# Kernel tuning notes

Hardware: AMD Instinct MI355X
Metric: run time of the kernel (lower is better)

Reference implementation:

```python
import jax, jax.numpy as jnp
import numpy as np

K = 20
NEG = 0.2      # leaky relu slope
EPS = 1e-5     # layernorm eps


def knn(x, k=K):
    # x: [B, C, N] -> neighbor indices [B, N, k] by largest negative sq-distance
    xt = jnp.swapaxes(x, 1, 2)                      # [B, N, C]
    inner = -2.0 * jnp.einsum('bnc,bcm->bnm', xt, x)
    xx = jnp.sum(x * x, axis=1)                     # [B, N]
    pd = -xx[:, :, None] - inner - xx[:, None, :]   # [B, N, N]
    _, idx = jax.lax.top_k(pd, k)
    return idx


def graph_feature(x, k=K):
    # x: [B, C, N] -> edge features [B, 2C, N, k] = cat(neighbor - center, center)
    xt = jnp.swapaxes(x, 1, 2)                      # [B, N, C]
    idx = knn(x, k)                                 # [B, N, k]
    nbr = jax.vmap(lambda f, i: f[i])(xt, idx)      # [B, N, k, C]
    ctr = jnp.broadcast_to(xt[:, :, None, :], nbr.shape)
    feat = jnp.concatenate([nbr - ctr, ctr], axis=-1)
    return jnp.transpose(feat, (0, 3, 1, 2))


def lrelu(x):
    return jnp.where(x >= 0, x, NEG * x)


def conv1x1(x, w):
    # x: [B, C, N, k], w: [O, C]  (BatchNorm2d in eval with default stats == identity)
    return jnp.einsum('oc,bcnk->bonk', w, x)


def layernorm(x, g, b):
    m = jnp.mean(x, axis=-1, keepdims=True)
    v = jnp.var(x, axis=-1, keepdims=True)
    return (x - m) * jax.lax.rsqrt(v + EPS) * g + b


def l2n(x):
    return x / jnp.linalg.norm(x, axis=1, keepdims=True)


def fc_layer(x, w, bias, g, beta):
    # l2-normalize -> Linear -> LayerNorm -> LeakyReLU (fc_layer with norm=True, bn=True)
    x = l2n(x)
    x = x @ w.T
    if bias is not None:
        x = x + bias
    return lrelu(layernorm(x, g, beta))


def transform_net(f0, tw1, tw2, tw3, tfc1_w, tfc1_g, tfc1_b, tfc2_w, tfc2_bias, tfc2_g, tfc2_b, tfc3_w, tfc3_b):
    # f0: [B, 6, N, k]
    h = lrelu(conv1x1(f0, tw1))                     # [B, 64, N, k]
    h = lrelu(conv1x1(h, tw2))                      # [B, 128, N, k]
    h = jnp.max(h, axis=-1, keepdims=True)          # [B, 128, N, 1]
    h = lrelu(conv1x1(h, tw3))                      # [B, 1024, N, 1]
    h = jnp.max(h, axis=2)[:, :, 0]                 # [B, 1024]
    h = fc_layer(h, tfc1_w, None, tfc1_g, tfc1_b)   # dgcnn: fc1 bias=False
    h = fc_layer(h, tfc2_w, tfc2_bias, tfc2_g, tfc2_b)
    h = h @ tfc3_w.T + tfc3_b                       # [B, 9]
    h = h + jnp.eye(3, dtype=h.dtype).reshape(9)
    return h.reshape(-1, 3, 3)


def setup_inputs() -> dict:
    key = jax.random.key(0)
    ks = jax.random.split(key, 16)

    def w(k, o, i):
        return jax.random.normal(k, (o, i), dtype=jnp.float32) / np.sqrt(i)

    inp = {
        'x': jax.random.normal(ks[0], (16, 3, 1024), dtype=jnp.float32),
        # transform_net params
        'tw1': w(ks[1], 64, 6),
        'tw2': w(ks[2], 128, 64),
        'tw3': w(ks[3], 1024, 128),
        'tfc1_w': w(ks[4], 512, 1024),
        'tfc1_g': jnp.ones((512,), jnp.float32),
        'tfc1_b': jnp.zeros((512,), jnp.float32),
        'tfc2_w': w(ks[5], 256, 512),
        'tfc2_bias': jnp.zeros((256,), jnp.float32),
        'tfc2_g': jnp.ones((256,), jnp.float32),
        'tfc2_b': jnp.zeros((256,), jnp.float32),
        'tfc3_w': w(ks[6], 9, 256) * 0.01,
        'tfc3_b': jnp.zeros((9,), jnp.float32),
        # EdgeConv params (1x1 convs, bias=False for dgcnn)
        'w1': w(ks[7], 64, 6),
        'w2': w(ks[8], 64, 128),
        'w3': w(ks[9], 128, 128),
        'w4': w(ks[10], 256, 256),
        'w5': w(ks[11], 1024, 512),
    }
    return inp


def reference(x, tw1, tw2, tw3, tfc1_w, tfc1_g, tfc1_b, tfc2_w, tfc2_bias, tfc2_g, tfc2_b,
              tfc3_w, tfc3_b, w1, w2, w3, w4, w5):
    # spatial transform from first graph feature
    f0 = graph_feature(x)                           # [B, 6, N, k]
    t = transform_net(f0, tw1, tw2, tw3, tfc1_w, tfc1_g, tfc1_b,
                      tfc2_w, tfc2_bias, tfc2_g, tfc2_b, tfc3_w, tfc3_b)
    x = jnp.einsum('bij,bjn->bin', t, x)            # [B, 3, N]

    # 4 EdgeConv blocks: graph_feature -> 1x1 conv (+BN identity) -> lrelu -> max over k
    x1 = jnp.max(lrelu(conv1x1(graph_feature(x), w1)), axis=-1)    # [B, 64, N]
    x2 = jnp.max(lrelu(conv1x1(graph_feature(x1), w2)), axis=-1)   # [B, 64, N]
    x3 = jnp.max(lrelu(conv1x1(graph_feature(x2), w3)), axis=-1)   # [B, 128, N]
    x4 = jnp.max(lrelu(conv1x1(graph_feature(x3), w4)), axis=-1)   # [B, 256, N]

    xc = jnp.concatenate([x1, x2, x3, x4], axis=1)  # [B, 512, N]
    x5 = lrelu(jnp.einsum('oc,bcn->bon', w5, xc))   # [B, 1024, N]
    return jnp.max(x5, axis=-1)                     # [B, 1024] global feature
```

## Files before the change

### kernel.cpp

```cpp
#include <hip/hip_runtime.h>
#include <math.h>

#define BATCH 16
#define NPTS 1024
#define KNN 20

__device__ __forceinline__ float lrelu(float v) { return v >= 0.f ? v : 0.2f * v; }

typedef __attribute__((ext_vector_type(8))) short bf16x8;
typedef __attribute__((ext_vector_type(4))) float f32x4;
typedef unsigned long long ull;

__device__ __forceinline__ ushort f2bf(float f) {
  union { float f; unsigned u; } v; v.f = f;
  unsigned r = (v.u + 0x7FFFu + ((v.u >> 16) & 1u)) >> 16;
  return (ushort)r;
}

__device__ __forceinline__ unsigned wave_min_u32(unsigned v) {
  unsigned t;
  t = (unsigned)__builtin_amdgcn_update_dpp((int)v, (int)v, 0x111, 0xf, 0xf, false);
  v = t < v ? t : v;
  t = (unsigned)__builtin_amdgcn_update_dpp((int)v, (int)v, 0x112, 0xf, 0xf, false);
  v = t < v ? t : v;
  t = (unsigned)__builtin_amdgcn_update_dpp((int)v, (int)v, 0x114, 0xf, 0xf, false);
  v = t < v ? t : v;
  t = (unsigned)__builtin_amdgcn_update_dpp((int)v, (int)v, 0x118, 0xf, 0xf, false);
  v = t < v ? t : v;
  t = (unsigned)__builtin_amdgcn_update_dpp((int)v, (int)v, 0x142, 0xf, 0xf, false);
  v = t < v ? t : v;
  t = (unsigned)__builtin_amdgcn_update_dpp((int)v, (int)v, 0x143, 0xf, 0xf, false);
  v = t < v ? t : v;
  return (unsigned)__builtin_amdgcn_readlane((int)v, 63);
}

__global__ __launch_bounds__(256)
void wsplit_t_kernel(const float* __restrict__ W, float* __restrict__ waT,
                     float* __restrict__ wdT, int O, int Cc) {
  int e = blockIdx.x * 256 + threadIdx.x;
  if (e < O * Cc) {
    int c = e / O, o = e - c * O;
    float a = W[o * 2 * Cc + c], bb = W[o * 2 * Cc + Cc + c];
    waT[e] = a; wdT[e] = bb - a;
  }
}

__global__ __launch_bounds__(256)
void wsplit_bf_kernel(const float* __restrict__ W, ushort* __restrict__ wa_bf,
                      ushort* __restrict__ wd_bf, int O, int Cc) {
  int e = blockIdx.x * 256 + threadIdx.x;
  if (e < O * Cc) {
    int o = e / Cc, c = e - o * Cc;
    float a = W[o * 2 * Cc + c], bb = W[o * 2 * Cc + Cc + c];
    wa_bf[e] = f2bf(a); wd_bf[e] = f2bf(bb - a);
  }
}

__global__ __launch_bounds__(256)
void cvt_bf16_kernel(const float* __restrict__ in, ushort* __restrict__ outp, int n) {
  int e = blockIdx.x * 256 + threadIdx.x;
  if (e < n) outp[e] = f2bf(in[e]);
}

__global__ __launch_bounds__(256)
void wtrans_kernel(const float* __restrict__ W, float* __restrict__ wT, int O, int Cc) {
  int e = blockIdx.x * 256 + threadIdx.x;
  if (e < O * Cc) {
    int c = e / O, o = e - c * O;
    wT[e] = W[(size_t)o * Cc + c];
  }
}

__global__ __launch_bounds__(256)
void xx3_kernel(const float* __restrict__ x, float* __restrict__ xx) {
  const int b = blockIdx.y;
  const int n = blockIdx.x * 256 + threadIdx.x;
  const float* xb = x + (size_t)b * 3 * NPTS;
  float a = xb[n], bb = xb[NPTS + n], c = xb[2 * NPTS + n];
  xx[b * NPTS + n] = a * a + bb * bb + c * c;
}

template<int C>
__global__ __launch_bounds__(256)
void knn_cn_kernel(const float* __restrict__ Xt, long sb,
                   const float* __restrict__ xx, int* __restrict__ idxout) {
  __shared__ float sc4[4][NPTS];
  const int b = blockIdx.y, i0 = blockIdx.x * 16;
  const int tid = threadIdx.x;
  const float* Xb = Xt + (size_t)b * sb;
  const int j0 = tid * 4;
  float acc[16][4];
  #pragma unroll
  for (int q = 0; q < 16; ++q)
    #pragma unroll
    for (int u = 0; u < 4; ++u) acc[q][u] = 0.f;
  for (int c = 0; c < C; ++c) {
    const float4 xv = *reinterpret_cast<const float4*>(Xb + (size_t)c * NPTS + j0);
    const float* xr = Xb + (size_t)c * NPTS + i0;
    #pragma unroll
    for (int q = 0; q < 16; ++q) {
      const float xiq = xr[q];
      acc[q][0] = fmaf(xiq, xv.x, acc[q][0]);
      acc[q][1] = fmaf(xiq, xv.y, acc[q][1]);
      acc[q][2] = fmaf(xiq, xv.z, acc[q][2]);
      acc[q][3] = fmaf(xiq, xv.w, acc[q][3]);
    }
  }
  const float4 xxj = *reinterpret_cast<const float4*>(xx + b * NPTS + j0);
  const int wv = tid >> 6, lane = tid & 63;
  unsigned ku[4][16];

  #pragma unroll
  for (int r = 0; r < 4; ++r) {
    if (r > 0) __syncthreads();
    #pragma unroll
    for (int q = 0; q < 4; ++q) {
      const int qq = r * 4 + q;
      float4 st;
      st.x = fmaf(-2.f, acc[qq][0], xxj.x);
      st.y = fmaf(-2.f, acc[qq][1], xxj.y);
      st.z = fmaf(-2.f, acc[qq][2], xxj.z);
      st.w = fmaf(-2.f, acc[qq][3], xxj.w);
      *reinterpret_cast<float4*>(&sc4[q][j0]) = st;
    }
    __syncthreads();
    #pragma unroll
    for (int s = 0; s < 16; ++s) {
      const unsigned u = __float_as_uint(sc4[wv][lane + 64 * s]);
      ku[r][s] = u ^ ((unsigned)((int)u >> 31) | 0x80000000u);
    }
  }

  unsigned c1s[4], c2s[4]; int c1j[4], c2j[4];
  #pragma unroll
  for (int r = 0; r < 4; ++r) {
    unsigned b1 = 0xFFFFFFFFu, b2 = 0xFFFFFFFFu; int s1 = 0, s2 = 0;
    #pragma unroll
    for (int s = 0; s < 16; ++s) {
      const unsigned k = ku[r][s];
      const bool a1 = k < b1, a2 = k < b2;
      const unsigned n1 = a1 ? k : b1;  const int ns1 = a1 ? s : s1;
      const unsigned n2 = a1 ? b1 : (a2 ? k : b2);
      const int ns2 = a1 ? s1 : (a2 ? s : s2);
      b1 = n1; s1 = ns1; b2 = n2; s2 = ns2;
    }
    c1s[r] = b1; c1j[r] = lane + (s1 << 6);
    c2s[r] = b2; c2j[r] = lane + (s2 << 6);
  }
  const unsigned INVS = 0xFFFFFFFFu;
  int my[4] = {0, 0, 0, 0};
  for (int t = 0; t < KNN; ++t) {
    unsigned ws[4]; int wl[4], jw[4];
    #pragma unroll
    for (int r = 0; r < 4; ++r) ws[r] = wave_min_u32(c1s[r]);
    #pragma unroll
    for (int r = 0; r < 4; ++r) wl[r] = __ffsll((long long)__ballot(c1s[r] == ws[r])) - 1;
    #pragma unroll
    for (int r = 0; r < 4; ++r) jw[r] = __builtin_amdgcn_readlane(c1j[r], wl[r]);
    if (lane == t) {
      #pragma unroll
      for (int r = 0; r < 4; ++r) my[r] = jw[r];
    }
    bool cons = false;
    #pragma unroll
    for (int r = 0; r < 4; ++r) {
      const bool win = (lane == wl[r]);
      c1s[r] = win ? c2s[r] : c1s[r];
      c1j[r] = win ? c2j[r] : c1j[r];
      c2s[r] = win ? INVS : c2s[r];
      cons = cons || (c1s[r] == INVS);
    }
    if (__any(cons)) {
      #pragma unroll
      for (int r = 0; r < 4; ++r) {
        if (c1s[r] == INVS) {
          unsigned m1 = INVS, m2 = INVS; int r1 = 0, r2 = 0;
          #pragma unroll
          for (int s = 0; s < 16; ++s) {
            const unsigned k = ku[r][s];
            const bool ok = k > ws[r];
            const bool a1 = ok && (k < m1), a2 = ok && (k < m2);
            const unsigned nm1 = a1 ? k : m1;  const int nr1 = a1 ? s : r1;
            const unsigned nm2 = a1 ? m1 : (a2 ? k : m2);
            const int nr2 = a1 ? r1 : (a2 ? s : r2);
            m1 = nm1; r1 = nr1; m2 = nm2; r2 = nr2;
          }
          c1s[r] = (m1 == INVS) ? 0xFFFFFFFEu : m1;  c1j[r] = lane + (r1 << 6);
          c2s[r] = (m2 == INVS) ? 0xFFFFFFFEu : m2;  c2j[r] = lane + (r2 << 6);
        }
      }
    }
  }
  if (lane < KNN) {
    #pragma unroll
    for (int r = 0; r < 4; ++r)
      idxout[(size_t)(b * NPTS + i0 + r * 4 + wv) * KNN + lane] = my[r];
  }
}

__global__ __launch_bounds__(256)
void gemm_dual_kernel(const float* __restrict__ X, long sxb, int sxn, int sxc,
                      const float* __restrict__ WaT, const float* __restrict__ WdT,
                      int ldW, int C,
                      float* __restrict__ outY, float* __restrict__ outZ,
                      int sob, int son) {
  __shared__ __align__(16) float Xs[16][64];
  __shared__ __align__(16) float Was[16][64];
  __shared__ __align__(16) float Wds[16][64];
  const int b = blockIdx.z;
  const int n0 = blockIdx.x * 64, o0 = blockIdx.y * 64;
  const int tid = threadIdx.x;
  const int lr = tid & 63;
  const int c4 = (tid >> 6) * 4;
  const int tn = tid & 15, to = tid >> 4;
  float accY[4][4], accZ[4][4];
  #pragma unroll
  for (int i = 0; i < 4; ++i)
    #pragma unroll
    for (int j = 0; j < 4; ++j) { accY[i][j] = 0.f; accZ[i][j] = 0.f; }

  const size_t xbase = (size_t)b * sxb;
  for (int k0 = 0; k0 < C; k0 += 16) {
    #pragma unroll
    for (int u = 0; u < 4; ++u) {
      int c = k0 + c4 + u;
      float xv = 0.f, wa = 0.f, wd = 0.f;
      if (c < C) {
        xv = X[xbase + (size_t)(n0 + lr) * sxn + (size_t)c * sxc];
        wa = WaT[(size_t)c * ldW + o0 + lr];
        wd = WdT[(size_t)c * ldW + o0 + lr];
      }
      Xs[c4 + u][lr] = xv;
      Was[c4 + u][lr] = wa;
      Wds[c4 + u][lr] = wd;
    }
    __syncthreads();
    #pragma unroll
    for (int kk = 0; kk < 16; ++kk) {
      const float4 xa = *reinterpret_cast<const float4*>(&Xs[kk][tn * 4]);
      const float4 wav = *reinterpret_cast<const float4*>(&Was[kk][to * 4]);
      const float4 wdv = *reinterpret_cast<const float4*>(&Wds[kk][to * 4]);
      const float xr[4] = {xa.x, xa.y, xa.z, xa.w};
      const float war[4] = {wav.x, wav.y, wav.z, wav.w};
      const float wdr[4] = {wdv.x, wdv.y, wdv.z, wdv.w};
      #pragma unroll
      for (int i = 0; i < 4; ++i)
        #pragma unroll
        for (int j = 0; j < 4; ++j) {
          accY[i][j] = fmaf(xr[i], war[j], accY[i][j]);
          accZ[i][j] = fmaf(xr[i], wdr[j], accZ[i][j]);
        }
    }
    __syncthreads();
  }
  #pragma unroll
  for (int i = 0; i < 4; ++i) {
    const size_t base = (size_t)b * sob + (size_t)(n0 + tn * 4 + i) * son + o0 + to * 4;
    *reinterpret_cast<float4*>(&outY[base]) =
      make_float4(accY[i][0], accY[i][1], accY[i][2], accY[i][3]);
    *reinterpret_cast<float4*>(&outZ[base]) =
      make_float4(accZ[i][0], accZ[i][1], accZ[i][2], accZ[i][3]);
  }
}

template<int EPI>
__global__ __launch_bounds__(256)
void gemm128_kernel(const float* __restrict__ X, long sxb, int scN,
                    const float* __restrict__ WT, int ldW, int C,
                    float* __restrict__ out, int sob, int son, int snb) {
  __shared__ __align__(16) float Xs[16][128];
  __shared__ __align__(16) float Ws[16][128];
  __shared__ __align__(16) float red[16][132];
  const int b = blockIdx.z;
  const int n0 = blockIdx.x * 128, o0 = blockIdx.y * 128;
  const int tid = threadIdx.x;
  const int tn = tid & 15, to = tid >> 4;
  float acc[8][8];
  #pragma unroll
  for (int i = 0; i < 8; ++i)
    #pragma unroll
    for (int j = 0; j < 8; ++j) acc[i][j] = 0.f;

  const size_t xbase = (size_t)b * sxb;
  for (int c0 = 0; c0 < C; c0 += 16) {
    #pragma unroll
    for (int it = 0; it < 2; ++it) {
      const int task = tid + it * 256;
      const int kk = task >> 5, n4 = (task & 31) * 4;
      *reinterpret_cast<float4*>(&Xs[kk][n4]) =
        *reinterpret_cast<const float4*>(&X[xbase + (size_t)(c0 + kk) * scN + n0 + n4]);
      *reinterpret_cast<float4*>(&Ws[kk][n4]) =
        *reinterpret_cast<const float4*>(&WT[(size_t)(c0 + kk) * ldW + o0 + n4]);
    }
    __syncthreads();
    #pragma unroll
    for (int kk = 0; kk < 16; ++kk) {
      const float4 xa0 = *reinterpret_cast<const float4*>(&Xs[kk][tn * 4]);
      const float4 xa1 = *reinterpret_cast<const float4*>(&Xs[kk][64 + tn * 4]);
      const float4 wb0 = *reinterpret_cast<const float4*>(&Ws[kk][to * 4]);
      const float4 wb1 = *reinterpret_cast<const float4*>(&Ws[kk][64 + to * 4]);
      const float xr[8] = {xa0.x, xa0.y, xa0.z, xa0.w, xa1.x, xa1.y, xa1.z, xa1.w};
      const float wr[8] = {wb0.x, wb0.y, wb0.z, wb0.w, wb1.x, wb1.y, wb1.z, wb1.w};
      #pragma unroll
      for (int i = 0; i < 8; ++i)
        #pragma unroll
        for (int j = 0; j < 8; ++j) acc[i][j] = fmaf(xr[i], wr[j], acc[i][j]);
    }
    __syncthreads();
  }

  if (EPI == 0) {
    #pragma unroll
    for (int i = 0; i < 8; ++i) {
      const int n = n0 + (i >> 2) * 64 + tn * 4 + (i & 3);
      float4 s0 = make_float4(acc[i][0], acc[i][1], acc[i][2], acc[i][3]);
      float4 s1 = make_float4(acc[i][4], acc[i][5], acc[i][6], acc[i][7]);
      *reinterpret_cast<float4*>(&out[(size_t)b * sob + (size_t)n * son + o0 + to * 4]) = s0;
      *reinterpret_cast<float4*>(&out[(size_t)b * sob + (size_t)n * son + o0 + 64 + to * 4]) = s1;
    }
  } else {
    #pragma unroll
    for (int j = 0; j < 8; ++j) {
      float m = lrelu(acc[0][j]);
      #pragma unroll
      for (int i = 1; i < 8; ++i) m = fmaxf(m, lrelu(acc[i][j]));
      red[tn][(j >> 2) * 64 + to * 4 + (j & 3)] = m;
    }
    __syncthreads();
    if (tid < 128) {
      float m = red[0][tid];
      #pragma unroll
      for (int t = 1; t < 16; ++t) m = fmaxf(m, red[t][tid]);
      out[(size_t)b * sob + (size_t)blockIdx.x * snb + o0 + tid] = m;
    }
  }
}

template<int EPI>
__global__ __launch_bounds__(256)
void gemm_mfma_kernel(const ushort* __restrict__ Xg, long sxb, int ldX,
                      const ushort* __restrict__ Wg, int ldW, int K,
                      float* __restrict__ out, long sob, int son, int snb) {
  __shared__ __align__(16) ushort As[128 * 64];
  __shared__ __align__(16) ushort Bs[128 * 64];
// ... 295 lines not shown
  }
  a2 = a2 * rinv2 + bias2[tid];
  float mean2 = block_reduce_sum(a2, rbuf) * (1.f / 256.f);
  float dd = a2 - mean2;
  float var2 = block_reduce_sum(dd * dd, rbuf) * (1.f / 256.f);
  float rs2 = 1.0f / sqrtf(var2 + 1e-5f);
  f2s[tid] = lrelu((a2 - mean2) * rs2 * g2[tid] + bb2[tid]);
  __syncthreads();
  if (tid < 9) {
    const float* wrow3 = Wt3 + tid * 256;
    float a3 = 0.f;
    for (int c = 0; c < 256; ++c) a3 = fmaf(wrow3[c], f2s[c], a3);
    a3 += bb3[tid];
    if (tid == 0 || tid == 4 || tid == 8) a3 += 1.f;
    tm[tid] = a3;
  }
  __syncthreads();
  const float* xb = x + (size_t)b * 3 * NPTS;
  float* ob = xt + (size_t)b * 3 * NPTS;
  #pragma unroll
  for (int nt = 0; nt < 4; ++nt) {
    const int n = nt * 256 + tid;
    const float x0 = xb[n], x1 = xb[NPTS + n], x2 = xb[2 * NPTS + n];
    #pragma unroll
    for (int i = 0; i < 3; ++i)
      ob[i * NPTS + n] = fmaf(tm[3 * i], x0, fmaf(tm[3 * i + 1], x1, tm[3 * i + 2] * x2));
  }
}

extern "C" void kernel_launch(void* const* d_in, const int* in_sizes, int n_in,
                              void* d_out, int out_size, void* d_ws, size_t ws_size,
                              hipStream_t stream) {
  (void)in_sizes; (void)n_in; (void)out_size; (void)ws_size;
  const float* x       = (const float*)d_in[0];
  const float* tw1     = (const float*)d_in[1];
  const float* tw2     = (const float*)d_in[2];
  const float* tw3     = (const float*)d_in[3];
  const float* tfc1_w  = (const float*)d_in[4];
  const float* tfc1_g  = (const float*)d_in[5];
  const float* tfc1_b  = (const float*)d_in[6];
  const float* tfc2_w  = (const float*)d_in[7];
  const float* tfc2_bias = (const float*)d_in[8];
  const float* tfc2_g  = (const float*)d_in[9];
  const float* tfc2_b  = (const float*)d_in[10];
  const float* tfc3_w  = (const float*)d_in[11];
  const float* tfc3_b  = (const float*)d_in[12];
  const float* w1      = (const float*)d_in[13];
  const float* w2      = (const float*)d_in[14];
  const float* w3      = (const float*)d_in[15];
  const float* w4      = (const float*)d_in[16];
  const float* w5      = (const float*)d_in[17];
  float* out = (float*)d_out;

  char* wsb = (char*)d_ws;
  size_t off = 0;
  auto alloc = [&](size_t bytes) -> void* {
    void* p = wsb + off;
    off += (bytes + 255) & ~(size_t)255;
    return p;
  };
  float* ybuf = (float*)alloc((size_t)BATCH * NPTS * 256 * 4);
  float* zbuf = (float*)alloc((size_t)BATCH * NPTS * 256 * 4);
  float* xcT  = (float*)alloc((size_t)BATCH * 512 * NPTS * 4);
  ushort* xc_bf = (ushort*)alloc((size_t)BATCH * NPTS * 512 * 2);
  float* h2m  = (float*)alloc((size_t)BATCH * 128 * NPTS * 4);
  float* part = (float*)alloc((size_t)BATCH * 16 * 1024 * 4);
  int*   idxb = (int*)alloc((size_t)BATCH * NPTS * KNN * 4);
  float* xxb  = (float*)alloc((size_t)BATCH * NPTS * 4);
  float* xt   = (float*)alloc((size_t)BATCH * 3 * NPTS * 4);
  float* tw1aT = (float*)alloc(3 * 64 * 4);
  float* tw1dT = (float*)alloc(3 * 64 * 4);
  float* w1aT  = (float*)alloc(3 * 64 * 4);
  float* w1dT  = (float*)alloc(3 * 64 * 4);
  float* w2aT  = (float*)alloc(64 * 64 * 4);
  float* w2dT  = (float*)alloc(64 * 64 * 4);
  float* w3aT  = (float*)alloc(64 * 128 * 4);
  float* w3dT  = (float*)alloc(64 * 128 * 4);
  ushort* w4a_bf = (ushort*)alloc(256 * 128 * 2);
  ushort* w4d_bf = (ushort*)alloc(256 * 128 * 2);
  ushort* w5_bf  = (ushort*)alloc(1024 * 512 * 2);
  float* tw2T  = (float*)alloc(64 * 128 * 4);
  float* tw3T  = (float*)alloc(128 * 1024 * 4);

  wsplit_t_kernel<<<1, 256, 0, stream>>>(tw1, tw1aT, tw1dT, 64, 3);
  wsplit_t_kernel<<<1, 256, 0, stream>>>(w1, w1aT, w1dT, 64, 3);
  wsplit_t_kernel<<<16, 256, 0, stream>>>(w2, w2aT, w2dT, 64, 64);
  wsplit_t_kernel<<<32, 256, 0, stream>>>(w3, w3aT, w3dT, 128, 64);
  wsplit_bf_kernel<<<128, 256, 0, stream>>>(w4, w4a_bf, w4d_bf, 256, 128);
  cvt_bf16_kernel<<<2048, 256, 0, stream>>>(w5, w5_bf, 1024 * 512);
  wtrans_kernel<<<32, 256, 0, stream>>>(tw2, tw2T, 128, 64);
  wtrans_kernel<<<512, 256, 0, stream>>>(tw3, tw3T, 1024, 128);

  xx3_kernel<<<dim3(4, 16), 256, 0, stream>>>(x, xxb);
  knn_cn_kernel<3><<<dim3(64, 16), 256, 0, stream>>>(x, 3 * NPTS, xxb, idxb);
  gemm_dual_kernel<<<dim3(16, 1, 16), 256, 0, stream>>>(x, 3 * NPTS, 1, NPTS, tw1aT, tw1dT,
                                                        64, 3, ybuf, zbuf, NPTS * 64, 64);
  h12_gemm_kernel<<<dim3(256, 16), 256, 0, stream>>>(ybuf, zbuf, idxb, tw2T, h2m);
  gemm128_kernel<1><<<dim3(8, 8, 16), 256, 0, stream>>>(h2m, 128 * NPTS, NPTS, tw3T, 1024, 128,
                                                        part, 8 * 1024, 0, 1024);
  fcall_kernel<<<16, 256, 0, stream>>>(part, tfc1_w, tfc1_g, tfc1_b,
                                       tfc2_w, tfc2_bias, tfc2_g, tfc2_b,
                                       tfc3_w, tfc3_b, x, xt);

  xx3_kernel<<<dim3(4, 16), 256, 0, stream>>>(xt, xxb);
  knn_cn_kernel<3><<<dim3(64, 16), 256, 0, stream>>>(xt, 3 * NPTS, xxb, idxb);
  gemm_dual_kernel<<<dim3(16, 1, 16), 256, 0, stream>>>(xt, 3 * NPTS, 1, NPTS, w1aT, w1dT,
                                                        64, 3, ybuf, zbuf, NPTS * 64, 64);
  edge_max_cn_kernel<64, 64><<<dim3(16, 16), 256, 0, stream>>>(ybuf, zbuf, idxb, xcT, xxb,
                                                               xc_bf, 0);

  knn_cn_kernel<64><<<dim3(64, 16), 256, 0, stream>>>(xcT, 512 * NPTS, xxb, idxb);
  gemm_dual_kernel<<<dim3(16, 1, 16), 256, 0, stream>>>(xcT, 512 * NPTS, 1, NPTS, w2aT, w2dT,
                                                        64, 64, ybuf, zbuf, NPTS * 64, 64);
  edge_max_cn_kernel<64, 64><<<dim3(16, 16), 256, 0, stream>>>(ybuf, zbuf, idxb,
                                                               xcT + 64 * NPTS, xxb, xc_bf, 64);

  knn_cn_kernel<64><<<dim3(64, 16), 256, 0, stream>>>(xcT + 64 * NPTS, 512 * NPTS, xxb, idxb);
  gemm_dual_kernel<<<dim3(16, 2, 16), 256, 0, stream>>>(xcT + 64 * NPTS, 512 * NPTS, 1, NPTS,
                                                        w3aT, w3dT, 128, 64,
                                                        ybuf, zbuf, NPTS * 128, 128);
  edge_max_cn_kernel<128, 64><<<dim3(16, 16), 256, 0, stream>>>(ybuf, zbuf, idxb,
                                                                xcT + 128 * NPTS, xxb, xc_bf, 128);

  knn_cn_kernel<128><<<dim3(64, 16), 256, 0, stream>>>(xcT + 128 * NPTS, 512 * NPTS, xxb, idxb);
  gemm_mfma_kernel<0><<<dim3(8, 2, 16), 256, 0, stream>>>(xc_bf + 128, (long)NPTS * 512, 512,
                                                          w4a_bf, 128, 128,
                                                          ybuf, (long)NPTS * 256, 256, 0);
  gemm_mfma_kernel<0><<<dim3(8, 2, 16), 256, 0, stream>>>(xc_bf + 128, (long)NPTS * 512, 512,
                                                          w4d_bf, 128, 128,
                                                          zbuf, (long)NPTS * 256, 256, 0);
  edge_max_cn_kernel<256, 32><<<dim3(32, 16), 256, 0, stream>>>(ybuf, zbuf, idxb,
                                                                xcT + 256 * NPTS, nullptr,
                                                                xc_bf, 256);

  gemm_mfma_kernel<1><<<dim3(8, 8, 16), 256, 0, stream>>>(xc_bf, (long)NPTS * 512, 512,
                                                          w5_bf, 512, 512,
                                                          part, 8 * 1024, 0, 1024);
  reduce_max_kernel<<<dim3(4, 16), 256, 0, stream>>>(part, out, 8);
}
```

Before: 734.9 us.

## Merge kNN and edge GEMM into single launches and fuse weight prep

Eight weight-preparation kernels become one prep_all_kernel. Each kNN launch and its independent dual-weight GEMM now share one launch, with block-index ranges deciding which work a block does, so the two run concurrently and launch count drops. For C=3 the squared norms are computed inside the kNN pass, which removes the xx3 kernels. This aims to cut launch overhead and fill the GPU better with the small GEMM grids, at the cost of heterogeneous blocks sharing one register and LDS allocation sized for the larger path.

Measured after the change: 690.1 us, median of 2. -6.1%, faster.

```diff
diff --git a/kernel.cpp b/kernel.cpp
--- a/kernel.cpp
+++ b/kernel.cpp
@@ -9,7 +9,6 @@
 
 typedef __attribute__((ext_vector_type(8))) short bf16x8;
 typedef __attribute__((ext_vector_type(4))) float f32x4;
-typedef unsigned long long ull;
 
 __device__ __forceinline__ ushort f2bf(float f) {
   union { float f; unsigned u; } v; v.f = f;
@@ -35,231 +34,437 @@
 }
 
 __global__ __launch_bounds__(256)
-void wsplit_t_kernel(const float* __restrict__ W, float* __restrict__ waT,
-                     float* __restrict__ wdT, int O, int Cc) {
-  int e = blockIdx.x * 256 + threadIdx.x;
-  if (e < O * Cc) {
-    int c = e / O, o = e - c * O;
-    float a = W[o * 2 * Cc + c], bb = W[o * 2 * Cc + Cc + c];
-    waT[e] = a; wdT[e] = bb - a;
-  }
-}
-
+void prep_all_kernel(const float* __restrict__ tw1, const float* __restrict__ w1,
+                     const float* __restrict__ w2, const float* __restrict__ w3,
+                     const float* __restrict__ w4, const float* __restrict__ w5,
+                     const float* __restrict__ tw2, const float* __restrict__ tw3,
+                     float* __restrict__ tw1aT, float* __restrict__ tw1dT,
+                     float* __restrict__ w1aT, float* __restrict__ w1dT,
+                     float* __restrict__ w2aT, float* __restrict__ w2dT,
+                     float* __restrict__ w3aT, float* __restrict__ w3dT,
+                     ushort* __restrict__ w4a_bf, ushort* __restrict__ w4d_bf,
+                     ushort* __restrict__ w5_bf,
+                     float* __restrict__ tw2T, float* __restrict__ tw3T) {
+  int g = blockIdx.x * 256 + threadIdx.x;
+  if (g < 524288) { w5_bf[g] = f2bf(w5[g]); return; }
+  g -= 524288;
+  if (g < 131072) { int c = g >> 10, o = g & 1023; tw3T[g] = tw3[o * 128 + c]; return; }
+  g -= 131072;
+  if (g < 32768) {
+    int o = g >> 7, c = g & 127;
+    float a = w4[o * 256 + c], bb = w4[o * 256 + 128 + c];
+    w4a_bf[g] = f2bf(a); w4d_bf[g] = f2bf(bb - a);
+    return;
+  }
+  g -= 32768;
+  if (g < 8192) {
+    int c = g >> 7, o = g & 127;
+    float a = w3[o * 128 + c], bb = w3[o * 128 + 64 + c];
+    w3aT[g] = a; w3dT[g] = bb - a;
+    return;
+  }
+  g -= 8192;
+  if (g < 8192) { int c = g >> 7, o = g & 127; tw2T[g] = tw2[o * 64 + c]; return; }
+  g -= 8192;
+  if (g < 4096) {
+    int c = g >> 6, o = g & 63;
+    float a = w2[o * 128 + c], bb = w2[o * 128 + 64 + c];
+    w2aT[g] = a; w2dT[g] = bb - a;
+    return;
+  }
+  g -= 4096;
+  if (g < 192) {
+    int c = g >> 6, o = g & 63;
+    float a = tw1[o * 6 + c], bb = tw1[o * 6 + 3 + c];
+    tw1aT[g] = a; tw1dT[g] = bb - a;
+    return;
+  }
+  g -= 192;
+  if (g < 192) {
+    int c = g >> 6, o = g & 63;
+    float a = w1[o * 6 + c], bb = w1[o * 6 + 3 + c];
+    w1aT[g] = a; w1dT[g] = bb - a;
+  }
+}
+
+template<int C, int NO>
 __global__ __launch_bounds__(256)
-void wsplit_bf_kernel(const float* __restrict__ W, ushort* __restrict__ wa_bf,
-                      ushort* __restrict__ wd_bf, int O, int Cc) {
-  int e = blockIdx.x * 256 + threadIdx.x;
-  if (e < O * Cc) {
-    int o = e / Cc, c = e - o * Cc;
-    float a = W[o * 2 * Cc + c], bb = W[o * 2 * Cc + Cc + c];
-    wa_bf[e] = f2bf(a); wd_bf[e] = f2bf(bb - a);
+void knn_dual_kernel(const float* __restrict__ X, long sxb,
+                     const float* __restrict__ xx, int* __restrict__ idxout,
+                     const float* __restrict__ WaT, const float* __restrict__ WdT,
+                     int ldW, float* __restrict__ outY, float* __restrict__ outZ,
+                     long sob, int son) {
+  __shared__ __align__(16) char smem[16384];
+  const int gid = blockIdx.x;
+  const int tid = threadIdx.x;
+
+  if (gid < 1024) {
+    float (*sc4)[NPTS] = reinterpret_cast<float (*)[NPTS]>(smem);
+    const int b = gid >> 6, i0 = (gid & 63) * 16;
+    const float* Xb = X + (size_t)b * sxb;
+    const int j0 = tid * 4;
+    float acc[16][4];
+    #pragma unroll
+    for (int q = 0; q < 16; ++q)
+      #pragma unroll
+      for (int u = 0; u < 4; ++u) acc[q][u] = 0.f;
+    float4 xxjv = make_float4(0.f, 0.f, 0.f, 0.f);
+    for (int c = 0; c < C; ++c) {
+      const float4 xv = *reinterpret_cast<const float4*>(Xb + (size_t)c * NPTS + j0);
+      if (C == 3) {
+        xxjv.x = fmaf(xv.x, xv.x, xxjv.x);
+        xxjv.y = fmaf(xv.y, xv.y, xxjv.y);
+        xxjv.z = fmaf(xv.z, xv.z, xxjv.z);
+        xxjv.w = fmaf(xv.w, xv.w, xxjv.w);
+      }
+      const float* xr = Xb + (size_t)c * NPTS + i0;
+      #pragma unroll
+      for (int q = 0; q < 16; ++q) {
+        const float xiq = xr[q];
+        acc[q][0] = fmaf(xiq, xv.x, acc[q][0]);
+        acc[q][1] = fmaf(xiq, xv.y, acc[q][1]);
+        acc[q][2] = fmaf(xiq, xv.z, acc[q][2]);
+        acc[q][3] = fmaf(xiq, xv.w, acc[q][3]);
+      }
+    }
+    float4 xxj;
+    if (C == 3) xxj = xxjv;
+    else xxj = *reinterpret_cast<const float4*>(xx + b * NPTS + j0);
+    const int wv = tid >> 6, lane = tid & 63;
+    unsigned ku[4][16];
+
+    #pragma unroll
+    for (int r = 0; r < 4; ++r) {
+      if (r > 0) __syncthreads();
+      #pragma unroll
+      for (int q = 0; q < 4; ++q) {
+        const int qq = r * 4 + q;
+        float4 st;
+        st.x = fmaf(-2.f, acc[qq][0], xxj.x);
+        st.y = fmaf(-2.f, acc[qq][1], xxj.y);
+        st.z = fmaf(-2.f, acc[qq][2], xxj.z);
+        st.w = fmaf(-2.f, acc[qq][3], xxj.w);
+        *reinterpret_cast<float4*>(&sc4[q][j0]) = st;
+      }
+      __syncthreads();
+      #pragma unroll
+      for (int s = 0; s < 16; ++s) {
+        const unsigned u = __float_as_uint(sc4[wv][lane + 64 * s]);
+        ku[r][s] = u ^ ((unsigned)((int)u >> 31) | 0x80000000u);
+      }
+    }
+
+    unsigned c1s[4], c2s[4]; int c1j[4], c2j[4];
+    #pragma unroll
+    for (int r = 0; r < 4; ++r) {
+      unsigned b1 = 0xFFFFFFFFu, b2 = 0xFFFFFFFFu; int s1 = 0, s2 = 0;
+      #pragma unroll
+      for (int s = 0; s < 16; ++s) {
+        const unsigned k = ku[r][s];
+        const bool a1 = k < b1, a2 = k < b2;
+        const unsigned n1 = a1 ? k : b1;  const int ns1 = a1 ? s : s1;
+        const unsigned n2 = a1 ? b1 : (a2 ? k : b2);
+        const int ns2 = a1 ? s1 : (a2 ? s : s2);
+        b1 = n1; s1 = ns1; b2 = n2; s2 = ns2;
+      }
+      c1s[r] = b1; c1j[r] = lane + (s1 << 6);
+      c2s[r] = b2; c2j[r] = lane + (s2 << 6);
+    }
+    const unsigned INVS = 0xFFFFFFFFu;
+    int my[4] = {0, 0, 0, 0};
+    for (int t = 0; t < KNN; ++t) {
+      unsigned ws[4]; int wl[4], jw[4];
+      #pragma unroll
+      for (int r = 0; r < 4; ++r) ws[r] = wave_min_u32(c1s[r]);
+      #pragma unroll
+      for (int r = 0; r < 4; ++r) wl[r] = __ffsll((long long)__ballot(c1s[r] == ws[r])) - 1;
+      #pragma unroll
+      for (int r = 0; r < 4; ++r) jw[r] = __builtin_amdgcn_readlane(c1j[r], wl[r]);
+      if (lane == t) {
+        #pragma unroll
+        for (int r = 0; r < 4; ++r) my[r] = jw[r];
+      }
+      bool cons = false;
+      #pragma unroll
+      for (int r = 0; r < 4; ++r) {
+        const bool win = (lane == wl[r]);
+        c1s[r] = win ? c2s[r] : c1s[r];
+        c1j[r] = win ? c2j[r] : c1j[r];
+        c2s[r] = win ? INVS : c2s[r];
+        cons = cons || (c1s[r] == INVS);
+      }
+      if (__any(cons)) {
+        #pragma unroll
+        for (int r = 0; r < 4; ++r) {
+          if (c1s[r] == INVS) {
+            unsigned m1 = INVS, m2 = INVS; int r1 = 0, r2 = 0;
+            #pragma unroll
+            for (int s = 0; s < 16; ++s) {
+              const unsigned k = ku[r][s];
+              const bool ok = k > ws[r];
+              const bool a1 = ok && (k < m1), a2 = ok && (k < m2);
+              const unsigned nm1 = a1 ? k : m1;  const int nr1 = a1 ? s : r1;
+              const unsigned nm2 = a1 ? m1 : (a2 ? k : m2);
+              const int nr2 = a1 ? r1 : (a2 ? s : r2);
+              m1 = nm1; r1 = nr1; m2 = nm2; r2 = nr2;
+            }
+            c1s[r] = (m1 == INVS) ? 0xFFFFFFFEu : m1;  c1j[r] = lane + (r1 << 6);
+            c2s[r] = (m2 == INVS) ? 0xFFFFFFFEu : m2;  c2j[r] = lane + (r2 << 6);
+          }
+        }
+      }
+    }
+    if (lane < KNN) {
+      #pragma unroll
+      for (int r = 0; r < 4; ++r)
+        idxout[(size_t)(b * NPTS + i0 + r * 4 + wv) * KNN + lane] = my[r];
+    }
+  } else {
+    float (*Xs)[64]  = reinterpret_cast<float (*)[64]>(smem);
+    float (*Was)[64] = reinterpret_cast<float (*)[64]>(smem + 4096);
+    float (*Wds)[64] = reinterpret_cast<float (*)[64]>(smem + 8192);
+    const int g2 = gid - 1024;
+    const int bx = g2 & 15;
+    const int rest = g2 >> 4;
+    const int oy = rest % NO;
+    const int b = rest / NO;
+    const int n0 = bx * 64, o0 = oy * 64;
+    const int lr = tid & 63;
+    const int c4 = (tid >> 6) * 4;
+    const int tn = tid & 15, to = tid >> 4;
+    float accY[4][4], accZ[4][4];
+    #pragma unroll
+    for (int i = 0; i < 4; ++i)
+      #pragma unroll
+      for (int j = 0; j < 4; ++j) { accY[i][j] = 0.f; accZ[i][j] = 0.f; }
+
+    const size_t xbase = (size_t)b * sxb;
+    for (int k0 = 0; k0 < C; k0 += 16) {
+      #pragma unroll
+      for (int u = 0; u < 4; ++u) {
+        int c = k0 + c4 + u;
+        float xv = 0.f, wa = 0.f, wd = 0.f;
+        if (c < C) {
+          xv = X[xbase + (size_t)(n0 + lr) + (size_t)c * NPTS];
+          wa = WaT[(size_t)c * ldW + o0 + lr];
+          wd = WdT[(size_t)c * ldW + o0 + lr];
+        }
+        Xs[c4 + u][lr] = xv;
+        Was[c4 + u][lr] = wa;
+        Wds[c4 + u][lr] = wd;
+      }
+      __syncthreads();
+      #pragma unroll
+      for (int kk = 0; kk < 16; ++kk) {
+        const float4 xa = *reinterpret_cast<const float4*>(&Xs[kk][tn * 4]);
+        const float4 wav = *reinterpret_cast<const float4*>(&Was[kk][to * 4]);
+        const float4 wdv = *reinterpret_cast<const float4*>(&Wds[kk][to * 4]);
+        const float xr[4] = {xa.x, xa.y, xa.z, xa.w};
+        const float war[4] = {wav.x, wav.y, wav.z, wav.w};
+        const float wdr[4] = {wdv.x, wdv.y, wdv.z, wdv.w};
+        #pragma unroll
+        for (int i = 0; i < 4; ++i)
+          #pragma unroll
+          for (int j = 0; j < 4; ++j) {
+            accY[i][j] = fmaf(xr[i], war[j], accY[i][j]);
+            accZ[i][j] = fmaf(xr[i], wdr[j], accZ[i][j]);
+          }
+      }
+      __syncthreads();
+    }
+    #pragma unroll
+    for (int i = 0; i < 4; ++i) {
+      const size_t base = (size_t)b * sob + (size_t)(n0 + tn * 4 + i) * son + o0 + to * 4;
+      *reinterpret_cast<float4*>(&outY[base]) =
+        make_float4(accY[i][0], accY[i][1], accY[i][2], accY[i][3]);
+      *reinterpret_cast<float4*>(&outZ[base]) =
+        make_float4(accZ[i][0], accZ[i][1], accZ[i][2], accZ[i][3]);
+    }
   }
 }
 
 __global__ __launch_bounds__(256)
-void cvt_bf16_kernel(const float* __restrict__ in, ushort* __restrict__ outp, int n) {
-  int e = blockIdx.x * 256 + threadIdx.x;
-  if (e < n) outp[e] = f2bf(in[e]);
-}
-
-__global__ __launch_bounds__(256)
-void wtrans_kernel(const float* __restrict__ W, float* __restrict__ wT, int O, int Cc) {
-  int e = blockIdx.x * 256 + threadIdx.x;
-  if (e < O * Cc) {
-    int c = e / O, o = e - c * O;
-    wT[e] = W[(size_t)o * Cc + c];
-  }
-}
-
-__global__ __launch_bounds__(256)
-void xx3_kernel(const float* __restrict__ x, float* __restrict__ xx) {
-  const int b = blockIdx.y;
-  const int n = blockIdx.x * 256 + threadIdx.x;
-  const float* xb = x + (size_t)b * 3 * NPTS;
-  float a = xb[n], bb = xb[NPTS + n], c = xb[2 * NPTS + n];
-  xx[b * NPTS + n] = a * a + bb * bb + c * c;
-}
-
-template<int C>
-__global__ __launch_bounds__(256)
-void knn_cn_kernel(const float* __restrict__ Xt, long sb,
-                   const float* __restrict__ xx, int* __restrict__ idxout) {
-  __shared__ float sc4[4][NPTS];
-  const int b = blockIdx.y, i0 = blockIdx.x * 16;
+void knn_mfma_kernel(const float* __restrict__ Xt, long sxb,
+                     const float* __restrict__ xx, int* __restrict__ idxout,
+                     const ushort* __restrict__ Xg,
+                     const ushort* __restrict__ w4a, const ushort* __restrict__ w4d,
+                     float* __restrict__ ybuf, float* __restrict__ zbuf) {
+  __shared__ __align__(16) char smem[32768];
+  const int gid = blockIdx.x;
   const int tid = threadIdx.x;
-  const float* Xb = Xt + (size_t)b * sb;
-  const int j0 = tid * 4;
-  float acc[16][4];
-  #pragma unroll
-  for (int q = 0; q < 16; ++q)
-    #pragma unroll
-    for (int u = 0; u < 4; ++u) acc[q][u] = 0.f;
-  for (int c = 0; c < C; ++c) {
-    const float4 xv = *reinterpret_cast<const float4*>(Xb + (size_t)c * NPTS + j0);
-    const float* xr = Xb + (size_t)c * NPTS + i0;
-    #pragma unroll
-    for (int q = 0; q < 16; ++q) {
-      const float xiq = xr[q];
-      acc[q][0] = fmaf(xiq, xv.x, acc[q][0]);
-      acc[q][1] = fmaf(xiq, xv.y, acc[q][1]);
-      acc[q][2] = fmaf(xiq, xv.z, acc[q][2]);
-      acc[q][3] = fmaf(xiq, xv.w, acc[q][3]);
-    }
-  }
-  const float4 xxj = *reinterpret_cast<const float4*>(xx + b * NPTS + j0);
-  const int wv = tid >> 6, lane = tid & 63;
-  unsigned ku[4][16];
-
-  #pragma unroll
-  for (int r = 0; r < 4; ++r) {
-    if (r > 0) __syncthreads();
-    #pragma unroll
-    for (int q = 0; q < 4; ++q) {
-      const int qq = r * 4 + q;
-      float4 st;
-      st.x = fmaf(-2.f, acc[qq][0], xxj.x);
-      st.y = fmaf(-2.f, acc[qq][1], xxj.y);
-      st.z = fmaf(-2.f, acc[qq][2], xxj.z);
-      st.w = fmaf(-2.f, acc[qq][3], xxj.w);
-      *reinterpret_cast<float4*>(&sc4[q][j0]) = st;
-    }
-    __syncthreads();
-    #pragma unroll
-    for (int s = 0; s < 16; ++s) {
-      const unsigned u = __float_as_uint(sc4[wv][lane + 64 * s]);
-      ku[r][s] = u ^ ((unsigned)((int)u >> 31) | 0x80000000u);
-    }
-  }
-
-  unsigned c1s[4], c2s[4]; int c1j[4], c2j[4];
-  #pragma unroll
-  for (int r = 0; r < 4; ++r) {
-    unsigned b1 = 0xFFFFFFFFu, b2 = 0xFFFFFFFFu; int s1 = 0, s2 = 0;
-    #pragma unroll
-    for (int s = 0; s < 16; ++s) {
-      const unsigned k = ku[r][s];
-      const bool a1 = k < b1, a2 = k < b2;
-      const unsigned n1 = a1 ? k : b1;  const int ns1 = a1 ? s : s1;
-      const unsigned n2 = a1 ? b1 : (a2 ? k : b2);
-      const int ns2 = a1 ? s1 : (a2 ? s : s2);
-      b1 = n1; s1 = ns1; b2 = n2; s2 = ns2;
-    }
-    c1s[r] = b1; c1j[r] = lane + (s1 << 6);
-    c2s[r] = b2; c2j[r] = lane + (s2 << 6);
-  }
-  const unsigned INVS = 0xFFFFFFFFu;
-  int my[4] = {0, 0, 0, 0};
-  for (int t = 0; t < KNN; ++t) {
-    unsigned ws[4]; int wl[4], jw[4];
-    #pragma unroll
-    for (int r = 0; r < 4; ++r) ws[r] = wave_min_u32(c1s[r]);
-    #pragma unroll
-    for (int r = 0; r < 4; ++r) wl[r] = __ffsll((long long)__ballot(c1s[r] == ws[r])) - 1;
-    #pragma unroll
-    for (int r = 0; r < 4; ++r) jw[r] = __builtin_amdgcn_readlane(c1j[r], wl[r]);
-    if (lane == t) {
-      #pragma unroll
-      for (int r = 0; r < 4; ++r) my[r] = jw[r];
-    }
-    bool cons = false;
+
+  if (gid < 1024) {
+    float (*sc4)[NPTS] = reinterpret_cast<float (*)[NPTS]>(smem);
+    const int b = gid >> 6, i0 = (gid & 63) * 16;
+    const float* Xb = Xt + (size_t)b * sxb;
+    const int j0 = tid * 4;
+    float acc[16][4];
+    #pragma unroll
+    for (int q = 0; q < 16; ++q)
+      #pragma unroll
+      for (int u = 0; u < 4; ++u) acc[q][u] = 0.f;
+    for (int c = 0; c < 128; ++c) {
+      const float4 xv = *reinterpret_cast<const float4*>(Xb + (size_t)c * NPTS + j0);
+      const float* xr = Xb + (size_t)c * NPTS + i0;
+      #pragma unroll
+      for (int q = 0; q < 16; ++q) {
+        const float xiq = xr[q];
+        acc[q][0] = fmaf(xiq, xv.x, acc[q][0]);
+        acc[q][1] = fmaf(xiq, xv.y, acc[q][1]);
+        acc[q][2] = fmaf(xiq, xv.z, acc[q][2]);
+        acc[q][3] = fmaf(xiq, xv.w, acc[q][3]);
+      }
+    }
+    const float4 xxj = *reinterpret_cast<const float4*>(xx + b * NPTS + j0);
+    const int wv = tid >> 6, lane = tid & 63;
+    unsigned ku[4][16];
     #pragma unroll
     for (int r = 0; r < 4; ++r) {
-      const bool win = (lane == wl[r]);
-      c1s[r] = win ? c2s[r] : c1s[r];
-      c1j[r] = win ? c2j[r] : c1j[r];
-      c2s[r] = win ? INVS : c2s[r];
-      cons = cons || (c1s[r] == INVS);
-    }
-    if (__any(cons)) {
+      if (r > 0) __syncthreads();
+      #pragma unroll
+      for (int q = 0; q < 4; ++q) {
+        const int qq = r * 4 + q;
+        float4 st;
+        st.x = fmaf(-2.f, acc[qq][0], xxj.x);
+        st.y = fmaf(-2.f, acc[qq][1], xxj.y);
+        st.z = fmaf(-2.f, acc[qq][2], xxj.z);
+        st.w = fmaf(-2.f, acc[qq][3], xxj.w);
+        *reinterpret_cast<float4*>(&sc4[q][j0]) = st;
+      }
+      __syncthreads();
+      #pragma unroll
+      for (int s = 0; s < 16; ++s) {
+        const unsigned u = __float_as_uint(sc4[wv][lane + 64 * s]);
+        ku[r][s] = u ^ ((unsigned)((int)u >> 31) | 0x80000000u);
+      }
+    }
+    unsigned c1s[4], c2s[4]; int c1j[4], c2j[4];
+    #pragma unroll
+    for (int r = 0; r < 4; ++r) {
+      unsigned b1 = 0xFFFFFFFFu, b2 = 0xFFFFFFFFu; int s1 = 0, s2 = 0;
+      #pragma unroll
+      for (int s = 0; s < 16; ++s) {
+        const unsigned k = ku[r][s];
+        const bool a1 = k < b1, a2 = k < b2;
+        const unsigned n1 = a1 ? k : b1;  const int ns1 = a1 ? s : s1;
+        const unsigned n2 = a1 ? b1 : (a2 ? k : b2);
+        const int ns2 = a1 ? s1 : (a2 ? s : s2);
+        b1 = n1; s1 = ns1; b2 = n2; s2 = ns2;
+      }
+      c1s[r] = b1; c1j[r] = lane + (s1 << 6);
+      c2s[r] = b2; c2j[r] = lane + (s2 << 6);
+    }
+    const unsigned INVS = 0xFFFFFFFFu;
+    int my[4] = {0, 0, 0, 0};
+    for (int t = 0; t < KNN; ++t) {
+      unsigned ws[4]; int wl[4], jw[4];
+      #pragma unroll
+      for (int r = 0; r < 4; ++r) ws[r] = wave_min_u32(c1s[r]);
+      #pragma unroll
+      for (int r = 0; r < 4; ++r) wl[r] = __ffsll((long long)__ballot(c1s[r] == ws[r])) - 1;
+      #pragma unroll
+      for (int r = 0; r < 4; ++r) jw[r] = __builtin_amdgcn_readlane(c1j[r], wl[r]);
+      if (lane == t) {
+        #pragma unroll
+        for (int r = 0; r < 4; ++r) my[r] = jw[r];
+      }
+      bool cons = false;
       #pragma unroll
       for (int r = 0; r < 4; ++r) {
-        if (c1s[r] == INVS) {
-          unsigned m1 = INVS, m2 = INVS; int r1 = 0, r2 = 0;
+        const bool win = (lane == wl[r]);
+        c1s[r] = win ? c2s[r] : c1s[r];
+        c1j[r] = win ? c2j[r] : c1j[r];
+        c2s[r] = win ? INVS : c2s[r];
+        cons = cons || (c1s[r] == INVS);
+      }
+      if (__any(cons)) {
+        #pragma unroll
+        for (int r = 0; r < 4; ++r) {
+          if (c1s[r] == INVS) {
+            unsigned m1 = INVS, m2 = INVS; int r1 = 0, r2 = 0;
+            #pragma unroll
+            for (int s = 0; s < 16; ++s) {
+              const unsigned k = ku[r][s];
+              const bool ok = k > ws[r];
+              const bool a1 = ok && (k < m1), a2 = ok && (k < m2);
+              const unsigned nm1 = a1 ? k : m1;  const int nr1 = a1 ? s : r1;
+              const unsigned nm2 = a1 ? m1 : (a2 ? k : m2);
+              const int nr2 = a1 ? r1 : (a2 ? s : r2);
+              m1 = nm1; r1 = nr1; m2 = nm2; r2 = nr2;
+            }
+            c1s[r] = (m1 == INVS) ? 0xFFFFFFFEu : m1;  c1j[r] = lane + (r1 << 6);
+            c2s[r] = (m2 == INVS) ? 0xFFFFFFFEu : m2;  c2j[r] = lane + (r2 << 6);
+          }
+        }
+      }
+    }
+    if (lane < KNN) {
+      #pragma unroll
+      for (int r = 0; r < 4; ++r)
+        idxout[(size_t)(b * NPTS + i0 + r * 4 + wv) * KNN + lane] = my[r];
+    }
+  } else {
+    char* As = smem;
+    char* Bs = smem + 16384;
+    int g2 = gid - 1024;
+    const ushort* Wg = (g2 < 256) ? w4a : w4d;
+    float* outp = (g2 < 256) ? ybuf : zbuf;
+    g2 &= 255;
+    const int bx = g2 & 7, oy = (g2 >> 3) & 1, b = g2 >> 4;
+    const int n0 = bx * 128, o0 = oy * 128;
+    const int lane = tid & 63;
+    const int wrow = (tid >> 6) >> 1, wcol = (tid >> 6) & 1;
+    f32x4 acc[4][4];
+    #pragma unroll
+    for (int i = 0; i < 4; ++i)
+      #pragma unroll
+      for (int j = 0; j < 4; ++j)
+        #pragma unroll
+        for (int r = 0; r < 4; ++r) acc[i][j][r] = 0.f;
+
+    const ushort* Xb = Xg + (size_t)b * NPTS * 512;
+    for (int kb = 0; kb < 128; kb += 64) {
+      #pragma unroll
+      for (int i = 0; i < 4; ++i) {
+        const int idx = i * 256 + tid;
+        const int n = idx >> 3, kc = idx & 7;
+        const bf16x8 xv = *reinterpret_cast<const bf16x8*>(&Xb[(size_t)(n0 + n) * 512 + kb + kc * 8]);
+        const bf16x8 wvv = *reinterpret_cast<const bf16x8*>(&Wg[(size_t)(o0 + n) * 128 + kb + kc * 8]);
+        const int ad = n * 128 + ((kc * 16) ^ ((n & 7) << 4));
+        *reinterpret_cast<bf16x8*>(As + ad) = xv;
+        *reinterpret_cast<bf16x8*>(Bs + ad) = wvv;
+      }
+      __syncthreads();
+      #pragma unroll
+      for (int s = 0; s < 2; ++s) {
+        bf16x8 af[4], bfr[4];
+        const int klane = (s * 64 + ((lane >> 4) << 4));
+        #pragma unroll
+        for (int f = 0; f < 4; ++f) {
+          const int nl = wrow * 64 + f * 16 + (lane & 15);
+          af[f] = *reinterpret_cast<const bf16x8*>(As + nl * 128 + (klane ^ ((nl & 7) << 4)));
+          const int ol = wcol * 64 + f * 16 + (lane & 15);
+          bfr[f] = *reinterpret_cast<const bf16x8*>(Bs + ol * 128 + (klane ^ ((ol & 7) << 4)));
+        }
+        #pragma unroll
+        for (int i = 0; i < 4; ++i)
           #pragma unroll
-          for (int s = 0; s < 16; ++s) {
-            const unsigned k = ku[r][s];
-            const bool ok = k > ws[r];
-            const bool a1 = ok && (k < m1), a2 = ok && (k < m2);
-            const unsigned nm1 = a1 ? k : m1;  const int nr1 = a1 ? s : r1;
-            const unsigned nm2 = a1 ? m1 : (a2 ? k : m2);
-            const int nr2 = a1 ? r1 : (a2 ? s : r2);
-            m1 = nm1; r1 = nr1; m2 = nm2; r2 = nr2;
-          }
-          c1s[r] = (m1 == INVS) ? 0xFFFFFFFEu : m1;  c1j[r] = lane + (r1 << 6);
-          c2s[r] = (m2 == INVS) ? 0xFFFFFFFEu : m2;  c2j[r] = lane + (r2 << 6);
+          for (int j = 0; j < 4; ++j)
+            acc[i][j] = __builtin_amdgcn_mfma_f32_16x16x32_bf16(af[i], bfr[j], acc[i][j], 0, 0, 0);
+      }
+      __syncthreads();
+    }
+    #pragma unroll
+    for (int i = 0; i < 4; ++i)
+      #pragma unroll
+      for (int r = 0; r < 4; ++r) {
+        const int n = n0 + wrow * 64 + i * 16 + ((lane >> 4) << 2) + r;
+        #pragma unroll
+        for (int j = 0; j < 4; ++j) {
+          const int o = o0 + wcol * 64 + j * 16 + (lane & 15);
+          outp[(size_t)b * NPTS * 256 + (size_t)n * 256 + o] = acc[i][j][r];
         }
       }
-    }
-  }
-  if (lane < KNN) {
-    #pragma unroll
-    for (int r = 0; r < 4; ++r)
-      idxout[(size_t)(b * NPTS + i0 + r * 4 + wv) * KNN + lane] = my[r];
-  }
-}
-
-__global__ __launch_bounds__(256)
-void gemm_dual_kernel(const float* __restrict__ X, long sxb, int sxn, int sxc,
-                      const float* __restrict__ WaT, const float* __restrict__ WdT,
-                      int ldW, int C,
-                      float* __restrict__ outY, float* __restrict__ outZ,
-                      int sob, int son) {
-  __shared__ __align__(16) float Xs[16][64];
-  __shared__ __align__(16) float Was[16][64];
-  __shared__ __align__(16) float Wds[16][64];
-  const int b = blockIdx.z;
-  const int n0 = blockIdx.x * 64, o0 = blockIdx.y * 64;
-  const int tid = threadIdx.x;
-  const int lr = tid & 63;
-  const int c4 = (tid >> 6) * 4;
-  const int tn = tid & 15, to = tid >> 4;
-  float accY[4][4], accZ[4][4];
-  #pragma unroll
-  for (int i = 0; i < 4; ++i)
-    #pragma unroll
-    for (int j = 0; j < 4; ++j) { accY[i][j] = 0.f; accZ[i][j] = 0.f; }
-
-  const size_t xbase = (size_t)b * sxb;
-  for (int k0 = 0; k0 < C; k0 += 16) {
-    #pragma unroll
-    for (int u = 0; u < 4; ++u) {
-      int c = k0 + c4 + u;
-      float xv = 0.f, wa = 0.f, wd = 0.f;
-      if (c < C) {
-        xv = X[xbase + (size_t)(n0 + lr) * sxn + (size_t)c * sxc];
-        wa = WaT[(size_t)c * ldW + o0 + lr];
-        wd = WdT[(size_t)c * ldW + o0 + lr];
-      }
-      Xs[c4 + u][lr] = xv;
-      Was[c4 + u][lr] = wa;
-      Wds[c4 + u][lr] = wd;
-    }
-    __syncthreads();
-    #pragma unroll
-    for (int kk = 0; kk < 16; ++kk) {
-      const float4 xa = *reinterpret_cast<const float4*>(&Xs[kk][tn * 4]);
-      const float4 wav = *reinterpret_cast<const float4*>(&Was[kk][to * 4]);
-      const float4 wdv = *reinterpret_cast<const float4*>(&Wds[kk][to * 4]);
-      const float xr[4] = {xa.x, xa.y, xa.z, xa.w};
-      const float war[4] = {wav.x, wav.y, wav.z, wav.w};
-      const float wdr[4] = {wdv.x, wdv.y, wdv.z, wdv.w};
-      #pragma unroll
-      for (int i = 0; i < 4; ++i)
-        #pragma unroll
-        for (int j = 0; j < 4; ++j) {
-          accY[i][j] = fmaf(xr[i], war[j], accY[i][j]);
-          accZ[i][j] = fmaf(xr[i], wdr[j], accZ[i][j]);
-        }
-    }
-    __syncthreads();
-  }
-  #pragma unroll
-  for (int i = 0; i < 4; ++i) {
-    const size_t base = (size_t)b * sob + (size_t)(n0 + tn * 4 + i) * son + o0 + to * 4;
-    *reinterpret_cast<float4*>(&outY[base]) =
-      make_float4(accY[i][0], accY[i][1], accY[i][2], accY[i][3]);
-    *reinterpret_cast<float4*>(&outZ[base]) =
-      make_float4(accZ[i][0], accZ[i][1], accZ[i][2], accZ[i][3]);
   }
 }
 
@@ -721,19 +926,14 @@
   float* tw2T  = (float*)alloc(64 * 128 * 4);
   float* tw3T  = (float*)alloc(128 * 1024 * 4);
 
-  wsplit_t_kernel<<<1, 256, 0, stream>>>(tw1, tw1aT, tw1dT, 64, 3);
-  wsplit_t_kernel<<<1, 256, 0, stream>>>(w1, w1aT, w1dT, 64, 3);
-  wsplit_t_kernel<<<16, 256, 0, stream>>>(w2, w2aT, w2dT, 64, 64);
-  wsplit_t_kernel<<<32, 256, 0, stream>>>(w3, w3aT, w3dT, 128, 64);
-  wsplit_bf_kernel<<<128, 256, 0, stream>>>(w4, w4a_bf, w4d_bf, 256, 128);
-  cvt_bf16_kernel<<<2048, 256, 0, stream>>>(w5, w5_bf, 1024 * 512);
-  wtrans_kernel<<<32, 256, 0, stream>>>(tw2, tw2T, 128, 64);
-  wtrans_kernel<<<512, 256, 0, stream>>>(tw3, tw3T, 1024, 128);
-
-  xx3_kernel<<<dim3(4, 16), 256, 0, stream>>>(x, xxb);
-  knn_cn_kernel<3><<<dim3(64, 16), 256, 0, stream>>>(x, 3 * NPTS, xxb, idxb);
-  gemm_dual_kernel<<<dim3(16, 1, 16), 256, 0, stream>>>(x, 3 * NPTS, 1, NPTS, tw1aT, tw1dT,
-                                                        64, 3, ybuf, zbuf, NPTS * 64, 64);
+  prep_all_kernel<<<2770, 256, 0, stream>>>(tw1, w1, w2, w3, w4, w5, tw2, tw3,
+                                            tw1aT, tw1dT, w1aT, w1dT, w2aT, w2dT,
+                                            w3aT, w3dT, w4a_bf, w4d_bf, w5_bf,
+                                            tw2T, tw3T);
+
+  knn_dual_kernel<3, 1><<<1280, 256, 0, stream>>>(x, 3 * NPTS, nullptr, idxb,
+                                                  tw1aT, tw1dT, 64,
+                                                  ybuf, zbuf, (long)NPTS * 64, 64);
   h12_gemm_kernel<<<dim3(256, 16), 256, 0, stream>>>(ybuf, zbuf, idxb, tw2T, h2m);
   gemm128_kernel<1><<<dim3(8, 8, 16), 256, 0, stream>>>(h2m, 128 * NPTS, NPTS, tw3T, 1024, 128,
                                                         part, 8 * 1024, 0, 1024);
@@ -741,33 +941,26 @@
                                        tfc2_w, tfc2_bias, tfc2_g, tfc2_b,
                                        tfc3_w, tfc3_b, x, xt);
 
-  xx3_kernel<<<dim3(4, 16), 256, 0, stream>>>(xt, xxb);
-  knn_cn_kernel<3><<<dim3(64, 16), 256, 0, stream>>>(xt, 3 * NPTS, xxb, idxb);
-  gemm_dual_kernel<<<dim3(16, 1, 16), 256, 0, stream>>>(xt, 3 * NPTS, 1, NPTS, w1aT, w1dT,
-                                                        64, 3, ybuf, zbuf, NPTS * 64, 64);
+  knn_dual_kernel<3, 1><<<1280, 256, 0, stream>>>(xt, 3 * NPTS, nullptr, idxb,
+                                                  w1aT, w1dT, 64,
+                                                  ybuf, zbuf, (long)NPTS * 64, 64);
   edge_max_cn_kernel<64, 64><<<dim3(16, 16), 256, 0, stream>>>(ybuf, zbuf, idxb, xcT, xxb,
                                                                xc_bf, 0);
 
-  knn_cn_kernel<64><<<dim3(64, 16), 256, 0, stream>>>(xcT, 512 * NPTS, xxb, idxb);
-  gemm_dual_kernel<<<dim3(16, 1, 16), 256, 0, stream>>>(xcT, 512 * NPTS, 1, NPTS, w2aT, w2dT,
-                                                        64, 64, ybuf, zbuf, NPTS * 64, 64);
+  knn_dual_kernel<64, 1><<<1280, 256, 0, stream>>>(xcT, 512 * NPTS, xxb, idxb,
+                                                   w2aT, w2dT, 64,
+                                                   ybuf, zbuf, (long)NPTS * 64, 64);
   edge_max_cn_kernel<64, 64><<<dim3(16, 16), 256, 0, stream>>>(ybuf, zbuf, idxb,
                                                                xcT + 64 * NPTS, xxb, xc_bf, 64);
 
-  knn_cn_kernel<64><<<dim3(64, 16), 256, 0, stream>>>(xcT + 64 * NPTS, 512 * NPTS, xxb, idxb);
-  gemm_dual_kernel<<<dim3(16, 2, 16), 256, 0, stream>>>(xcT + 64 * NPTS, 512 * NPTS, 1, NPTS,
-                                                        w3aT, w3dT, 128, 64,
-                                                        ybuf, zbuf, NPTS * 128, 128);
+  knn_dual_kernel<64, 2><<<1536, 256, 0, stream>>>(xcT + 64 * NPTS, 512 * NPTS, xxb, idxb,
+                                                   w3aT, w3dT, 128,
+                                                   ybuf, zbuf, (long)NPTS * 128, 128);
   edge_max_cn_kernel<128, 64><<<dim3(16, 16), 256, 0, stream>>>(ybuf, zbuf, idxb,
                                                                 xcT + 128 * NPTS, xxb, xc_bf, 128);
 
-  knn_cn_kernel<128><<<dim3(64, 16), 256, 0, stream>>>(xcT + 128 * NPTS, 512 * NPTS, xxb, idxb);
-  gemm_mfma_kernel<0><<<dim3(8, 2, 16), 256, 0, stream>>>(xc_bf + 128, (long)NPTS * 512, 512,
-                                                          w4a_bf, 128, 128,
-                                                          ybuf, (long)NPTS * 256, 256, 0);
-  gemm_mfma_kernel<0><<<dim3(8, 2, 16), 256, 0, stream>>>(xc_bf + 128, (long)NPTS * 512, 512,
-                                                          w4d_bf, 128, 128,
-                                                          zbuf, (long)NPTS * 256, 256, 0);
+  knn_mfma_kernel<<<1536, 256, 0, stream>>>(xcT + 128 * NPTS, 512 * NPTS, xxb, idxb,
+                                            xc_bf + 128, w4a_bf, w4d_bf, ybuf, zbuf);
   edge_max_cn_kernel<256, 32><<<dim3(32, 16), 256, 0, stream>>>(ybuf, zbuf, idxb,
                                                                 xcT + 256 * NPTS, nullptr,
                                                                 xc_bf, 256);
```
